# Kernel optimization log

Hardware: AMD Instinct MI355X
Metric: run time of the kernel (lower is better)

## Reference

```python
import jax, jax.numpy as jnp
import numpy as np


def setup_inputs() -> dict:
    key = jax.random.key(0)
    k1, k2 = jax.random.split(key)
    B, N, M, D = 4, 8192, 8192, 3
    pred = jax.random.normal(k1, (B, N, D), dtype=jnp.float32)
    target = jax.random.normal(k2, (B, M, D), dtype=jnp.float32)
    return {"pred": pred, "target": target}


def reference(pred, target):
    # Pairwise squared distances via the GEMM cross-term trick:
    # ||p - t||^2 = ||p||^2 + ||t||^2 - 2 <p, t>
    pn = jnp.sum(pred * pred, axis=-1)            # [B, N]
    tn = jnp.sum(target * target, axis=-1)        # [B, M]
    cross = jnp.einsum('bnd,bmd->bnm', pred, target)  # [B, N, M]
    dist = pn[:, :, None] + tn[:, None, :] - 2.0 * cross
    d_pt = jnp.min(dist, axis=2)  # [B, N] pred -> nearest target
    d_tp = jnp.min(dist, axis=1)  # [B, M] target -> nearest pred
    return jnp.mean(d_pt) + jnp.mean(d_tp)
```

## Files before the change

### kernel.cpp

```cpp
#include <hip/hip_runtime.h>
#include <hip/hip_bf16.h>


typedef __attribute__((ext_vector_type(8)))  short short8;
typedef __attribute__((ext_vector_type(16))) float f32x16;

#define BATCH 4
#define NPTS 8192
#define TOTALQ (BATCH * NPTS)
#define BLK 256
#define WNT 4
#define BCOLS 512
#define MSPLIT 8
#define MC (NPTS / MSPLIT)
#define MT_PER (MC / 32)

__device__ __forceinline__ unsigned short f2bf(float f) {
    unsigned int u = __float_as_uint(f);
    u += 0x7FFFu + ((u >> 16) & 1u);
    return (unsigned short)(u >> 16);
}
__device__ __forceinline__ float bf2f(unsigned short h) {
    return __uint_as_float(((unsigned int)h) << 16);
}
__device__ __forceinline__ unsigned int pk2(unsigned short a, unsigned short b) {
    return (unsigned int)a | ((unsigned int)b << 16);
}

struct Payload {
    unsigned short hx, hy, hz, lx, ly, lz, n1, n2, n3;
};
__device__ __forceinline__ Payload split_point(float x, float y, float z) {
    Payload P;
    P.hx = f2bf(x);  P.hy = f2bf(y);  P.hz = f2bf(z);
    P.lx = f2bf(x - bf2f(P.hx));
    P.ly = f2bf(y - bf2f(P.hy));
    P.lz = f2bf(z - bf2f(P.hz));
    float nrm = fmaf(z, z, fmaf(y, y, x * x));
    P.n1 = f2bf(nrm);
    float r1 = nrm - bf2f(P.n1);
    P.n2 = f2bf(r1);
    P.n3 = f2bf(r1 - bf2f(P.n2));
    return P;
}

__global__ __launch_bounds__(BLK) void chamfer_mega_kernel(
        const float* __restrict__ pred, const float* __restrict__ target,
        float* __restrict__ part, float* __restrict__ out)
{
    const int dir = blockIdx.z;
    const float* __restrict__ Q  = dir ? target : pred;
    const float* __restrict__ Tg = dir ? pred : target;

    const int nch = blockIdx.x;
    const int b   = nch >> 4;
    const int ms  = blockIdx.y;
    const int w    = threadIdx.x >> 6;
    const int lane = threadIdx.x & 63;
    const int c = lane & 31;
    const int g = lane >> 5;
    const unsigned short ONE = 0x3F80;

    if (blockIdx.x == 0 && blockIdx.y == 0 && blockIdx.z == 0 &&
        threadIdx.x == 0) out[0] = 0.0f;

    __shared__ uint4 ldsb[2][MC];

    #pragma unroll
    for (int j = 0; j < MC / BLK; ++j) {
        int p = j * BLK + threadIdx.x;
        size_t gp = (size_t)b * NPTS + (size_t)ms * MC + p;
        float x = Tg[3 * gp], y = Tg[3 * gp + 1], z = Tg[3 * gp + 2];
        Payload P = split_point(x, y, z);
        ldsb[0][p] = (uint4){ pk2(P.hx, P.hy), pk2(P.hz, P.hx),
                              pk2(P.hy, P.hz), pk2(P.lx, P.ly) };
        ldsb[1][p] = (uint4){ pk2(P.lz, ONE), pk2(ONE, ONE),
                              pk2(P.n1, P.n2), pk2(P.n3, 0) };
    }

    const int colstart = nch * BCOLS + w * (WNT * 32);
    short8 bq[WNT];
    #pragma unroll
    for (int nt = 0; nt < WNT; ++nt) {
        int r = colstart + nt * 32 + c;
        float x = Q[3 * r], y = Q[3 * r + 1], z = Q[3 * r + 2];
        Payload P = split_point(x, y, z);
        unsigned short ax = f2bf(-2.f * bf2f(P.hx)),
                       ay = f2bf(-2.f * bf2f(P.hy)),
                       az = f2bf(-2.f * bf2f(P.hz));
        unsigned short cx = f2bf(-2.f * bf2f(P.lx)),
                       cy = f2bf(-2.f * bf2f(P.ly)),
                       cz = f2bf(-2.f * bf2f(P.lz));
        uint4 h0 = { pk2(ax, ay), pk2(az, cx), pk2(cy, cz), pk2(ax, ay) };
        uint4 h1 = { pk2(az, P.n1), pk2(P.n2, P.n3), pk2(ONE, ONE), pk2(ONE, 0) };
        uint4 sel = g ? h1 : h0;
        bq[nt] = *(short8*)&sel;
    }

    f32x16 acc[WNT];
    #pragma unroll
    for (int nt = 0; nt < WNT; ++nt)
        #pragma unroll
        for (int r = 0; r < 16; ++r) acc[nt][r] = 3.4e38f;

    f32x16 vzero;
    #pragma unroll
    for (int r = 0; r < 16; ++r) vzero[r] = 0.0f;

    __syncthreads();

    const ushort* ldsu = (const ushort*)&ldsb[g][0];

    #pragma unroll 2
    for (int mt = 0; mt < MT_PER; mt += 2) {
        short8 at0 = *(const short8*)(ldsu + (mt * 32 + c) * 8);
        short8 at1 = *(const short8*)(ldsu + ((mt + 1) * 32 + c) * 8);
        #pragma unroll
        for (int nt = 0; nt < WNT; ++nt) {
            f32x16 d0 = __builtin_amdgcn_mfma_f32_32x32x16_bf16(
                            at0, bq[nt], vzero, 0, 0, 0);
            f32x16 d1 = __builtin_amdgcn_mfma_f32_32x32x16_bf16(
                            at1, bq[nt], vzero, 0, 0, 0);
            #pragma unroll
            for (int r = 0; r < 16; ++r)
                acc[nt][r] = fminf(fminf(acc[nt][r], d0[r]), d1[r]);
        }
    }

    float* rp = part + (size_t)(dir * MSPLIT + ms) * TOTALQ;
    #pragma unroll
    for (int nt = 0; nt < WNT; ++nt) {
        f32x16 v = acc[nt];
        float m0 = fminf(fminf(v[0],  v[1]),  fminf(v[2],  v[3]));
        float m1 = fminf(fminf(v[4],  v[5]),  fminf(v[6],  v[7]));
        float m2 = fminf(fminf(v[8],  v[9]),  fminf(v[10], v[11]));
        float m3 = fminf(fminf(v[12], v[13]), fminf(v[14], v[15]));
        float m  = fminf(fminf(m0, m1), fminf(m2, m3));
        m = fminf(m, __shfl_xor(m, 32, 64));
        if (g == 0) rp[colstart + nt * 32 + c] = m;
    }
}

__global__ __launch_bounds__(BLK) void chamfer_reduce_kernel(
        const float* __restrict__ part, float* __restrict__ out)
{
    int gl = blockIdx.x * BLK + threadIdx.x;
    int dir = gl >> 15, i = gl & (TOTALQ - 1);

    const float* p = part + (size_t)dir * MSPLIT * TOTALQ + i;
    float m = p[0];
    #pragma unroll
    for (int s = 1; s < MSPLIT; ++s)
        m = fminf(m, p[(size_t)s * TOTALQ]);

    float acc = m * (1.0f / (float)TOTALQ);
    #pragma unroll
    for (int off = 32; off > 0; off >>= 1)
        acc += __shfl_down(acc, off, 64);
    __shared__ float wsum[BLK / 64];
    int lane = threadIdx.x & 63, wid = threadIdx.x >> 6;
    if (lane == 0) wsum[wid] = acc;
    __syncthreads();
    if (threadIdx.x == 0) {
        float s = 0.0f;
        #pragma unroll
        for (int wv = 0; wv < BLK / 64; ++wv) s += wsum[wv];
        atomicAdd(out, s);
    }
}

extern "C" void kernel_launch(void* const* d_in, const int* in_sizes, int n_in,
                              void* d_out, int out_size, void* d_ws, size_t ws_size,
                              hipStream_t stream) {
    const float* pred   = (const float*)d_in[0];
    const float* target = (const float*)d_in[1];
    float*       out    = (float*)d_out;
    float*       part   = (float*)d_ws;

    dim3 grid(TOTALQ / BCOLS, MSPLIT, 2);
    hipLaunchKernelGGL(chamfer_mega_kernel, grid, dim3(BLK), 0, stream,
                       pred, target, part, out);

    hipLaunchKernelGGL(chamfer_reduce_kernel, dim3(2 * TOTALQ / BLK), dim3(BLK),
                       0, stream, (const float*)part, out);
}
```

Before: 83.29 us.

## Software-pipeline MFMA with fminf reduction using inline asm and sched barriers

Replaces the compiler-scheduled MFMA+min loop with a hand-pipelined sequence: each pair of MFMAs, issued via inline asm, runs while the VALU min-reduction consumes the previous tile's results, using double-buffered result registers (p/q). Sched barriers pin the ordering so the MFMA latency is hidden behind the fminf work. The first iteration's min over the initial 3.4e38 p buffers is harmless, and a trailing min drains the last tile. Inline asm hides hazard info from the compiler, and the loop unroll drops to 1, which adds loop overhead.

```diff
diff --git a/kernel.cpp b/kernel.cpp
--- a/kernel.cpp
+++ b/kernel.cpp
@@ -44,6 +44,17 @@
     return P;
 }
 
+#define MFMA2(D0, D1, A0, A1, BQ)                              \
+    asm("v_mfma_f32_32x32x16_bf16 %0, %2, %4, %5\n\t"          \
+        "v_mfma_f32_32x32x16_bf16 %1, %3, %4, %5"              \
+        : "=&v"(D0), "=&v"(D1)                                 \
+        : "v"(A0), "v"(A1), "v"(BQ), "v"(vzero))
+
+#define MIN16(NT, D0, D1)                                      \
+    _Pragma("unroll")                                          \
+    for (int r = 0; r < 16; ++r)                               \
+        acc[NT][r] = fminf(fminf(acc[NT][r], (D0)[r]), (D1)[r])
+
 __global__ __launch_bounds__(BLK) void chamfer_mega_kernel(
         const float* __restrict__ pred, const float* __restrict__ target,
         float* __restrict__ part, float* __restrict__ out)
@@ -107,25 +118,36 @@
     #pragma unroll
     for (int r = 0; r < 16; ++r) vzero[r] = 0.0f;
 
+    f32x16 p0, p1, q0, q1;
+    #pragma unroll
+    for (int r = 0; r < 16; ++r) { p0[r] = 3.4e38f; p1[r] = 3.4e38f; }
+
     __syncthreads();
 
     const ushort* ldsu = (const ushort*)&ldsb[g][0];
 
-    #pragma unroll 2
+    #pragma unroll 1
     for (int mt = 0; mt < MT_PER; mt += 2) {
         short8 at0 = *(const short8*)(ldsu + (mt * 32 + c) * 8);
         short8 at1 = *(const short8*)(ldsu + ((mt + 1) * 32 + c) * 8);
-        #pragma unroll
-        for (int nt = 0; nt < WNT; ++nt) {
-            f32x16 d0 = __builtin_amdgcn_mfma_f32_32x32x16_bf16(
-                            at0, bq[nt], vzero, 0, 0, 0);
-            f32x16 d1 = __builtin_amdgcn_mfma_f32_32x32x16_bf16(
-                            at1, bq[nt], vzero, 0, 0, 0);
-            #pragma unroll
-            for (int r = 0; r < 16; ++r)
-                acc[nt][r] = fminf(fminf(acc[nt][r], d0[r]), d1[r]);
-        }
-    }
+
+        MFMA2(q0, q1, at0, at1, bq[0]);
+        __builtin_amdgcn_sched_barrier(0);
+        MIN16(3, p0, p1);
+
+        MFMA2(p0, p1, at0, at1, bq[1]);
+        __builtin_amdgcn_sched_barrier(0);
+        MIN16(0, q0, q1);
+
+        MFMA2(q0, q1, at0, at1, bq[2]);
+        __builtin_amdgcn_sched_barrier(0);
+        MIN16(1, p0, p1);
+
+        MFMA2(p0, p1, at0, at1, bq[3]);
+        __builtin_amdgcn_sched_barrier(0);
+        MIN16(2, q0, q1);
+    }
+    MIN16(3, p0, p1);
 
     float* rp = part + (size_t)(dir * MSPLIT + ms) * TOTALQ;
     #pragma unroll
```

Result: faster. 77.52 us (-6.9%).
